# Kernel tuning notes

Hardware: AMD Instinct MI355X
Metric: run time of the kernel (lower is better)

The kernel has to match this reference:

```python
import jax, jax.numpy as jnp
import numpy as np

B, S, D, H = 1, 2048, 1024, 16
HD = D // H  # head_dim = 64
ROPE_BASE = 10000.0


def setup_inputs() -> dict:
    key = jax.random.key(0)
    k1, k2, k3, k4, k5 = jax.random.split(key, 5)
    std = 0.02
    return {
        "hidden_states": jax.random.normal(k1, (B, S, D), dtype=jnp.float32),
        "attention_mask": jnp.ones((B, S), dtype=jnp.int32),
        "position_ids": jnp.broadcast_to(jnp.arange(S, dtype=jnp.int32), (B, S)),
        "wq": jax.random.normal(k2, (D, D), dtype=jnp.float32) * std,
        "wk": jax.random.normal(k3, (D, D), dtype=jnp.float32) * std,
        "wv": jax.random.normal(k4, (D, D), dtype=jnp.float32) * std,
        "wo": jax.random.normal(k5, (D, D), dtype=jnp.float32) * std,
    }


def _rope_cos_sin(position_ids):
    # standard llama freqs: 1/base^(2i/hd), interleaved-pair rotation
    inv_freq = 1.0 / (ROPE_BASE ** (jnp.arange(0, HD, 2, dtype=jnp.float32) / HD))  # [HD/2]
    freqs = position_ids.astype(jnp.float32)[..., None] * inv_freq  # [B,S,HD/2]
    # add head axis for broadcasting: [B,S,1,HD/2]
    return jnp.cos(freqs)[:, :, None, :], jnp.sin(freqs)[:, :, None, :]


def _apply_rope(x, cos, sin):
    # x: [B,S,H,HD]; pairs (x0,x1) rotated as complex (x0+i*x1)*(cos+i*sin)
    x2 = x.reshape(x.shape[:-1] + (HD // 2, 2))
    x0, x1 = x2[..., 0], x2[..., 1]
    out = jnp.stack([x0 * cos - x1 * sin, x0 * sin + x1 * cos], axis=-1)
    return out.reshape(x.shape)


def _attention(hidden_states, attention_mask, position_ids, wq, wk, wv, wo):
    xq = (hidden_states @ wq).reshape(B, S, H, HD)
    xk = (hidden_states @ wk).reshape(B, S, H, HD)
    xv = (hidden_states @ wv).reshape(B, S, H, HD)

    cos, sin = _rope_cos_sin(position_ids)
    xq = _apply_rope(xq, cos, sin)
    xk = _apply_rope(xk, cos, sin)

    # combined causal + padding mask -> additive bias
    causal = jnp.tril(jnp.ones((S, S), dtype=bool))[None, None]  # [1,1,S,S]
    pad = (attention_mask > 0)[:, None, None, :]  # [B,1,1,S]
    mask = jnp.logical_and(causal, pad)
    neg = jnp.finfo(jnp.float32).min
    bias = jnp.where(mask, 0.0, neg).astype(jnp.float32)

    scale = 1.0 / np.sqrt(HD).astype(np.float32)
    scores = jnp.einsum("bqhd,bkhd->bhqk", xq, xk) * scale + bias  # [B,H,S,S]
    attn_weights = jax.nn.softmax(scores, axis=-1)

    attn_output = jnp.einsum("bhqk,bkhd->bqhd", attn_weights, xv)
    attn_output = attn_output.reshape(B, S, D)
    return attn_output @ wo


def reference(hidden_states, attention_mask, position_ids, wq, wk, wv, wo):
    return _attention(hidden_states, attention_mask, position_ids, wq, wk, wv, wo)
```

## Files before the change

kernel.cpp:

```cpp
#include <hip/hip_runtime.h>
#include <stdint.h>

#define SEQ 2048
#define DMODEL 1024
#define NHEAD 16
#define HDIM 64
#define KCH 256
#define NCH 8
#define NITEMS 576
#define WPH 512

typedef unsigned short u16;
typedef __attribute__((ext_vector_type(4))) float f32x4;
typedef __attribute__((ext_vector_type(8))) __bf16 bf16x8;
typedef __attribute__((ext_vector_type(8))) u16 u16x8;

__device__ __forceinline__ u16 f2bf(float f) {
  unsigned int u = __builtin_bit_cast(unsigned int, f);
  unsigned int r = (u + 0x7FFFu + ((u >> 16) & 1u)) >> 16;
  return (u16)r;
}
__device__ __forceinline__ float bf2f(u16 b) {
  unsigned int u = ((unsigned int)b) << 16;
  return __builtin_bit_cast(float, u);
}
__device__ __forceinline__ bf16x8 load8(const u16* p) {
  return __builtin_bit_cast(bf16x8, *(const u16x8*)p);
}
__device__ __forceinline__ void gl_lds16(const void* g, void* l) {
  __builtin_amdgcn_global_load_lds(
      (const __attribute__((address_space(1))) unsigned int*)g,
      (__attribute__((address_space(3))) unsigned int*)l, 16, 0, 0);
}

__global__ __launch_bounds__(256) void convert_x(const float* __restrict__ X,
                                                 u16* __restrict__ Xb) {
  int i = (blockIdx.x * 256 + threadIdx.x) * 4;
  float4 v = *(const float4*)(X + i);
  union { u16 s[4]; uint2 u; } o;
  o.s[0] = f2bf(v.x); o.s[1] = f2bf(v.y); o.s[2] = f2bf(v.z); o.s[3] = f2bf(v.w);
  *(uint2*)(Xb + i) = o.u;
}

__global__ __launch_bounds__(256) void transpose_w(
    const float* __restrict__ W0, const float* __restrict__ W1,
    const float* __restrict__ W2, const float* __restrict__ W3,
    u16* __restrict__ T0, u16* __restrict__ T1,
    u16* __restrict__ T2, u16* __restrict__ T3) {
  __shared__ u16 tile[64][65];
  int bz = blockIdx.z;
  const float* W = bz == 0 ? W0 : bz == 1 ? W1 : bz == 2 ? W2 : W3;
  u16* T = bz == 0 ? T0 : bz == 1 ? T1 : bz == 2 ? T2 : T3;
  int n0 = blockIdx.x * 64, k0 = blockIdx.y * 64;
  int t = threadIdx.x;
#pragma unroll 4
  for (int i = 0; i < 16; ++i) {
    int idx = i * 256 + t;
    int r = idx >> 6, c = idx & 63;
    tile[r][c] = f2bf(W[(k0 + r) * 1024 + n0 + c]);
  }
  __syncthreads();
#pragma unroll 4
  for (int i = 0; i < 16; ++i) {
    int idx = i * 256 + t;
    int r = idx >> 6, c = idx & 63;
    T[(n0 + r) * 1024 + k0 + c] = tile[c][r];
  }
}

template <int BM, int BN, int NMATS, bool OUTF32>
__global__ __launch_bounds__(256) void gemm_bf16(
    const u16* __restrict__ A, const u16* __restrict__ B0,
    const u16* __restrict__ B1, const u16* __restrict__ B2,
    u16* __restrict__ O0, u16* __restrict__ O1, u16* __restrict__ O2,
    float* __restrict__ OF) {
  constexpr int MI = BM / 32, NI = BN / 32;
  constexpr int LA = BM / 64, LB = BN / 64;
  __shared__ u16 As[BM * 32];
  __shared__ u16 Bs[BN * 32];
  const int t = threadIdx.x;
  const int lane = t & 63, w = t >> 6;
  const int g = lane >> 4, li = lane & 15;
  const int n0g = blockIdx.x * BN;
  const int mat = n0g >> 10;
  const int n0 = n0g & 1023;
  const u16* Bp = (NMATS == 1 || mat == 0) ? B0 : (mat == 1 ? B1 : B2);
  const int m0 = blockIdx.y * BM;
  const int wm = (w >> 1) * (BM / 2), wn = (w & 1) * (BN / 2);
  f32x4 acc[MI][NI] = {};
  for (int k0 = 0; k0 < 1024; k0 += 32) {
#pragma unroll
    for (int it = 0; it < LA; ++it) {
      int L = it * 2048 + t * 8;
      int r = L >> 5, c = L & 31;
      gl_lds16(A + (m0 + r) * 1024 + k0 + c, (char*)As + it * 4096 + w * 1024);
    }
#pragma unroll
    for (int it = 0; it < LB; ++it) {
      int L = it * 2048 + t * 8;
      int r = L >> 5, c = L & 31;
      gl_lds16(Bp + (n0 + r) * 1024 + k0 + c, (char*)Bs + it * 4096 + w * 1024);
    }
    __syncthreads();
    bf16x8 af[MI], bfr[NI];
#pragma unroll
    for (int mi = 0; mi < MI; ++mi) af[mi] = load8(&As[(wm + mi * 16 + li) * 32 + g * 8]);
#pragma unroll
    for (int ni = 0; ni < NI; ++ni) bfr[ni] = load8(&Bs[(wn + ni * 16 + li) * 32 + g * 8]);
#pragma unroll
    for (int mi = 0; mi < MI; ++mi)
#pragma unroll
      for (int ni = 0; ni < NI; ++ni)
        acc[mi][ni] = __builtin_amdgcn_mfma_f32_16x16x32_bf16(af[mi], bfr[ni], acc[mi][ni], 0, 0, 0);
    __syncthreads();
  }
  u16* Ob = (NMATS == 1 || mat == 0) ? O0 : (mat == 1 ? O1 : O2);
#pragma unroll
  for (int mi = 0; mi < MI; ++mi)
#pragma unroll
    for (int ni = 0; ni < NI; ++ni)
#pragma unroll
      for (int r = 0; r < 4; ++r) {
        int m = m0 + wm + mi * 16 + g * 4 + r;
        int n = n0 + wn + ni * 16 + li;
        float v = acc[mi][ni][r];
        if (OUTF32) OF[m * 1024 + n] = v;
        else Ob[m * 1024 + n] = f2bf(v);
      }
}

__global__ __launch_bounds__(256) void rope_qk(u16* __restrict__ Qb, u16* __restrict__ Kb,
                                               const int* __restrict__ pos_ids) {
  int gid = blockIdx.x * 256 + threadIdx.x;
  int s = gid >> 9;
  int rem = gid & 511;
  int h = rem >> 5, i = rem & 31;
  float pos = (float)pos_ids[s];
  float inv = exp2f(-(float)i * (13.287712379549449f / 32.0f));
  float ang = pos * inv;
  float sn, cs;
  sincosf(ang, &sn, &cs);
  int base = s * 1024 + h * 64 + 2 * i;
  {
    float x0 = bf2f(Qb[base]), x1 = bf2f(Qb[base + 1]);
    Qb[base]     = f2bf((x0 * cs - x1 * sn) * 0.125f);
    Qb[base + 1] = f2bf((x0 * sn + x1 * cs) * 0.125f);
  }
  {
    float x0 = bf2f(Kb[base]), x1 = bf2f(Kb[base + 1]);
    Kb[base]     = f2bf(x0 * cs - x1 * sn);
    Kb[base + 1] = f2bf(x0 * sn + x1 * cs);
  }
}

__global__ __launch_bounds__(256) void v_transpose(const u16* __restrict__ Vb,
                                                   u16* __restrict__ Vt) {
  __shared__ u16 tile[64][65];
  const int t = threadIdx.x;
  const int s0 = blockIdx.x * 64, h = blockIdx.y;
#pragma unroll 4
  for (int i = 0; i < 16; ++i) {
    int idx = i * 256 + t;
    int r = idx >> 6, c = idx & 63;
    tile[r][c] = Vb[(s0 + r) * 1024 + h * 64 + c];
  }
  __syncthreads();
#pragma unroll 4
  for (int i = 0; i < 16; ++i) {
    int idx = i * 256 + t;
    int d = idx >> 6, sc = idx & 63;
    Vt[h * (64 * 2048) + d * 2048 + s0 + sc] = tile[sc][d];
  }
}

__global__ __launch_bounds__(256) void attn_partial(
    const u16* __restrict__ Qb, const u16* __restrict__ Kb,
    const u16* __restrict__ Vt, const int* __restrict__ amask,
    float* __restrict__ Mpart, float* __restrict__ Lpart, u16* __restrict__ Opart) {
  const int t = threadIdx.x, lane = t & 63, w = t >> 6;
  const int g = lane >> 4, li = lane & 15;
  const int bid = blockIdx.x;
  const int h = bid & 15;
  const int wih = (bid >> 4) * 4 + w;
  __shared__ u16 Plds[4][16][40];
  const u16* Vh = Vt + h * (64 * 2048);
  for (int j = wih; j < NITEMS; j += WPH) {
    int c = (j >= 560) ? 7 : (j >= 528) ? 6 : (j >= 480) ? 5 : (j >= 416) ? 4
          : (j >= 336) ? 3 : (j >= 240) ? 2 : (j >= 128) ? 1 : 0;
    int qb = 16 * c + (j - (128 * c - 8 * c * (c - 1)));
    const int qb16 = qb * 16;
    const int kstart = c * KCH;
    const int kend = min(kstart + KCH, qb16 + 16);
    bf16x8 qf0 = load8(Qb + (qb16 + li) * 1024 + h * 64 + 0 + g * 8);
    bf16x8 qf1 = load8(Qb + (qb16 + li) * 1024 + h * 64 + 32 + g * 8);
    f32x4 acc[4] = {};
    float mrow[4] = {-1e30f, -1e30f, -1e30f, -1e30f};
    float lrow[4] = {0.f, 0.f, 0.f, 0.f};
    for (int k0 = kstart; k0 < kend; k0 += 32) {
      f32x4 sc[2] = {};
#pragma unroll
      for (int sub = 0; sub < 2; ++sub) {
        bf16x8 kf0 = load8(Kb + (k0 + sub * 16 + li) * 1024 + h * 64 + 0 + g * 8);
        bf16x8 kf1 = load8(Kb + (k0 + sub * 16 + li) * 1024 + h * 64 + 32 + g * 8);
        sc[sub] = __builtin_amdgcn_mfma_f32_16x16x32_bf16(qf0, kf0, sc[sub], 0, 0, 0);
        sc[sub] = __builtin_amdgcn_mfma_f32_16x16x32_bf16(qf1, kf1, sc[sub], 0, 0, 0);
      }
      float sv[2][4];
      float tmax[4] = {-1e30f, -1e30f, -1e30f, -1e30f};
#pragma unroll
      for (int sub = 0; sub < 2; ++sub) {
        int key = k0 + sub * 16 + li;
        bool kok = (amask[key] != 0);
#pragma unroll
        for (int r = 0; r < 4; ++r) {
          int q = qb16 + g * 4 + r;
          float v = (kok && key <= q) ? sc[sub][r] : -1e30f;
          sv[sub][r] = v;
          tmax[r] = fmaxf(tmax[r], v);
        }
      }
#pragma unroll
      for (int m = 1; m < 16; m <<= 1)
#pragma unroll
        for (int r = 0; r < 4; ++r) tmax[r] = fmaxf(tmax[r], __shfl_xor(tmax[r], m, 64));
      float alpha[4];
#pragma unroll
      for (int r = 0; r < 4; ++r) {
        float mn = fmaxf(mrow[r], tmax[r]);
        alpha[r] = __expf(mrow[r] - mn);
        mrow[r] = mn;
      }
      float ps[4] = {0.f, 0.f, 0.f, 0.f};
#pragma unroll
      for (int sub = 0; sub < 2; ++sub)
#pragma unroll
        for (int r = 0; r < 4; ++r) {
          float p = __expf(sv[sub][r] - mrow[r]);
          ps[r] += p;
          Plds[w][g * 4 + r][sub * 16 + li] = f2bf(p);
        }
#pragma unroll
      for (int m = 1; m < 16; m <<= 1)
#pragma unroll
        for (int r = 0; r < 4; ++r) ps[r] += __shfl_xor(ps[r], m, 64);
#pragma unroll
      for (int r = 0; r < 4; ++r) lrow[r] = lrow[r] * alpha[r] + ps[r];
#pragma unroll
      for (int ti = 0; ti < 4; ++ti)
#pragma unroll
        for (int r = 0; r < 4; ++r) acc[ti][r] *= alpha[r];
      bf16x8 pf = load8(&Plds[w][li][g * 8]);
#pragma unroll
      for (int ti = 0; ti < 4; ++ti) {
        bf16x8 vf = load8(Vh + (ti * 16 + li) * 2048 + k0 + g * 8);
        acc[ti] = __builtin_amdgcn_mfma_f32_16x16x32_bf16(pf, vf, acc[ti], 0, 0, 0);
      }
    }
    const int idx = (h * 128 + qb) * NCH + c;
    if (li == 0) {
#pragma unroll
      for (int r = 0; r < 4; ++r) {
        Mpart[idx * 16 + g * 4 + r] = mrow[r];
        Lpart[idx * 16 + g * 4 + r] = lrow[r];
      }
    }
#pragma unroll
    for (int ti = 0; ti < 4; ++ti)
#pragma unroll
      for (int r = 0; r < 4; ++r)
        Opart[idx * 1024 + (g * 4 + r) * 64 + ti * 16 + li] = f2bf(acc[ti][r]);
  }
}

__global__ __launch_bounds__(256) void attn_combine(
    const float* __restrict__ Mpart, const float* __restrict__ Lpart,
    const u16* __restrict__ Opart, u16* __restrict__ Ab) {
  const int qb = blockIdx.x, h = blockIdx.y;
  const int t = threadIdx.x;
  const int q = t >> 4, dg = t & 15;
  const int nch = qb / 16 + 1;
  const int base = (h * 128 + qb) * NCH;
  float M = -1e30f;
#pragma unroll
  for (int c = 0; c < NCH; ++c)
    if (c < nch) M = fmaxf(M, Mpart[(base + c) * 16 + q]);
  float L = 0.f;
  float o[4] = {0.f, 0.f, 0.f, 0.f};
#pragma unroll
  for (int c = 0; c < NCH; ++c)
    if (c < nch) {
      float e = __expf(Mpart[(base + c) * 16 + q] - M);
      L += e * Lpart[(base + c) * 16 + q];
      const u16* op = Opart + (base + c) * 1024 + q * 64 + dg * 4;
      uint2 pk = *(const uint2*)op;
      const u16* ps = (const u16*)&pk;
#pragma unroll
      for (int j = 0; j < 4; ++j) o[j] += e * bf2f(ps[j]);
    }
  float inv = 1.f / L;
  u16* dst = Ab + (qb * 16 + q) * 1024 + h * 64 + dg * 4;
  union { u16 s[4]; uint2 u; } ou;
#pragma unroll
  for (int j = 0; j < 4; ++j) ou.s[j] = f2bf(o[j] * inv);
  *(uint2*)dst = ou.u;
}

extern "C" void kernel_launch(void* const* d_in, const int* in_sizes, int n_in,
                              void* d_out, int out_size, void* d_ws, size_t ws_size,
                              hipStream_t stream) {
  const float* X = (const float*)d_in[0];
  const int* amask = (const int*)d_in[1];
  const int* pos = (const int*)d_in[2];
  const float* wq = (const float*)d_in[3];
  const float* wk = (const float*)d_in[4];
  const float* wv = (const float*)d_in[5];
  const float* wo = (const float*)d_in[6];
  float* out = (float*)d_out;
  char* ws = (char*)d_ws;
  u16* Xb  = (u16*)(ws);
  u16* Wtq = (u16*)(ws + (4u  << 20));
  u16* Wtk = (u16*)(ws + (6u  << 20));
  u16* Wtv = (u16*)(ws + (8u  << 20));
  u16* Wto = (u16*)(ws + (10u << 20));
  u16* Qb  = (u16*)(ws + (12u << 20));
  u16* Kb  = (u16*)(ws + (16u << 20));
  u16* Vb  = (u16*)(ws + (20u << 20));
  u16* Vt  = (u16*)(ws + (24u << 20));
  u16* Ab  = (u16*)(ws + (28u << 20));
  float* Mpart = (float*)(ws + (32u << 20));
  float* Lpart = (float*)(ws + (33u << 20));
  u16*   Opart = (u16*)(ws + (34u << 20));

  convert_x<<<2048, 256, 0, stream>>>(X, Xb);
  transpose_w<<<dim3(16, 16, 4), 256, 0, stream>>>(wq, wk, wv, wo, Wtq, Wtk, Wtv, Wto);
  gemm_bf16<64, 128, 3, false><<<dim3(24, 32), 256, 0, stream>>>(Xb, Wtq, Wtk, Wtv, Qb, Kb, Vb, nullptr);
  rope_qk<<<4096, 256, 0, stream>>>(Qb, Kb, pos);
  v_transpose<<<dim3(32, 16), 256, 0, stream>>>(Vb, Vt);
  attn_partial<<<2048, 256, 0, stream>>>(Qb, Kb, Vt, amask, Mpart, Lpart, Opart);
  attn_combine<<<dim3(128, 16), 256, 0, stream>>>(Mpart, Lpart, Opart, Ab);
  gemm_bf16<64, 64, 1, true><<<dim3(16, 32), 256, 0, stream>>>(Ab, Wto, nullptr, nullptr,
                                                               nullptr, nullptr, nullptr, out);
}
```

Measured before the change: 145.6 us.

## Widen attention work items to 32 queries and 64-key steps for K/V reuse

```diff
diff --git a/kernel.cpp b/kernel.cpp
--- a/kernel.cpp
+++ b/kernel.cpp
@@ -7,8 +7,7 @@
 #define HDIM 64
 #define KCH 256
 #define NCH 8
-#define NITEMS 576
-#define WPH 512
+#define NIT32 288
 
 typedef unsigned short u16;
 typedef __attribute__((ext_vector_type(4))) float f32x4;
@@ -181,95 +180,136 @@
   const int g = lane >> 4, li = lane & 15;
   const int bid = blockIdx.x;
   const int h = bid & 15;
-  const int wih = (bid >> 4) * 4 + w;
-  __shared__ u16 Plds[4][16][40];
+  const int j = (bid >> 4) * 4 + w;
+  __shared__ u16 Plds[4][2][16][72];
   const u16* Vh = Vt + h * (64 * 2048);
-  for (int j = wih; j < NITEMS; j += WPH) {
-    int c = (j >= 560) ? 7 : (j >= 528) ? 6 : (j >= 480) ? 5 : (j >= 416) ? 4
-          : (j >= 336) ? 3 : (j >= 240) ? 2 : (j >= 128) ? 1 : 0;
-    int qb = 16 * c + (j - (128 * c - 8 * c * (c - 1)));
-    const int qb16 = qb * 16;
-    const int kstart = c * KCH;
-    const int kend = min(kstart + KCH, qb16 + 16);
-    bf16x8 qf0 = load8(Qb + (qb16 + li) * 1024 + h * 64 + 0 + g * 8);
-    bf16x8 qf1 = load8(Qb + (qb16 + li) * 1024 + h * 64 + 32 + g * 8);
-    f32x4 acc[4] = {};
-    float mrow[4] = {-1e30f, -1e30f, -1e30f, -1e30f};
-    float lrow[4] = {0.f, 0.f, 0.f, 0.f};
-    for (int k0 = kstart; k0 < kend; k0 += 32) {
-      f32x4 sc[2] = {};
-#pragma unroll
-      for (int sub = 0; sub < 2; ++sub) {
-        bf16x8 kf0 = load8(Kb + (k0 + sub * 16 + li) * 1024 + h * 64 + 0 + g * 8);
-        bf16x8 kf1 = load8(Kb + (k0 + sub * 16 + li) * 1024 + h * 64 + 32 + g * 8);
-        sc[sub] = __builtin_amdgcn_mfma_f32_16x16x32_bf16(qf0, kf0, sc[sub], 0, 0, 0);
-        sc[sub] = __builtin_amdgcn_mfma_f32_16x16x32_bf16(qf1, kf1, sc[sub], 0, 0, 0);
-      }
-      float sv[2][4];
-      float tmax[4] = {-1e30f, -1e30f, -1e30f, -1e30f};
-#pragma unroll
-      for (int sub = 0; sub < 2; ++sub) {
-        int key = k0 + sub * 16 + li;
-        bool kok = (amask[key] != 0);
+  const int c = (j >= 280) ? 7 : (j >= 264) ? 6 : (j >= 240) ? 5 : (j >= 208) ? 4
+              : (j >= 168) ? 3 : (j >= 120) ? 2 : (j >= 64) ? 1 : 0;
+  const int qb = 8 * c + (j - (64 * c - 4 * c * (c - 1)));
+  const int q0 = qb * 32;
+  const int kstart = c * KCH;
+  const int kend = min(kstart + KCH, q0 + 32);
+  bf16x8 qf[2][2];
+#pragma unroll
+  for (int a = 0; a < 2; ++a)
+#pragma unroll
+    for (int hf = 0; hf < 2; ++hf)
+      qf[a][hf] = load8(Qb + (q0 + a * 16 + li) * 1024 + h * 64 + hf * 32 + g * 8);
+  f32x4 acc[2][4] = {};
+  float mrow[2][4], lrow[2][4];
+#pragma unroll
+  for (int a = 0; a < 2; ++a)
+#pragma unroll
+    for (int r = 0; r < 4; ++r) { mrow[a][r] = -1e30f; lrow[a][r] = 0.f; }
+  for (int k0 = kstart; k0 < kend; k0 += 64) {
+    f32x4 sc[2][4] = {};
+#pragma unroll
+    for (int s = 0; s < 4; ++s) {
+      bf16x8 kf0 = load8(Kb + (k0 + s * 16 + li) * 1024 + h * 64 + 0 + g * 8);
+      bf16x8 kf1 = load8(Kb + (k0 + s * 16 + li) * 1024 + h * 64 + 32 + g * 8);
+#pragma unroll
+      for (int a = 0; a < 2; ++a) {
+        sc[a][s] = __builtin_amdgcn_mfma_f32_16x16x32_bf16(qf[a][0], kf0, sc[a][s], 0, 0, 0);
+        sc[a][s] = __builtin_amdgcn_mfma_f32_16x16x32_bf16(qf[a][1], kf1, sc[a][s], 0, 0, 0);
+      }
+    }
+    float sv[2][4][4];
+    float tmax[2][4];
+#pragma unroll
+    for (int a = 0; a < 2; ++a)
+#pragma unroll
+      for (int r = 0; r < 4; ++r) tmax[a][r] = -1e30f;
+#pragma unroll
+    for (int s = 0; s < 4; ++s) {
+      int key = k0 + s * 16 + li;
+      bool kok = (amask[key] != 0);
+#pragma unroll
+      for (int a = 0; a < 2; ++a)
 #pragma unroll
         for (int r = 0; r < 4; ++r) {
-          int q = qb16 + g * 4 + r;
-          float v = (kok && key <= q) ? sc[sub][r] : -1e30f;
-          sv[sub][r] = v;
-          tmax[r] = fmaxf(tmax[r], v);
+          int q = q0 + a * 16 + g * 4 + r;
+          float v = (kok && key <= q) ? sc[a][s][r] : -1e30f;
+          sv[a][s][r] = v;
+          tmax[a][r] = fmaxf(tmax[a][r], v);
         }
-      }
-#pragma unroll
-      for (int m = 1; m < 16; m <<= 1)
-#pragma unroll
-        for (int r = 0; r < 4; ++r) tmax[r] = fmaxf(tmax[r], __shfl_xor(tmax[r], m, 64));
-      float alpha[4];
+    }
+#pragma unroll
+    for (int m = 1; m < 16; m <<= 1)
+#pragma unroll
+      for (int a = 0; a < 2; ++a)
+#pragma unroll
+        for (int r = 0; r < 4; ++r)
+          tmax[a][r] = fmaxf(tmax[a][r], __shfl_xor(tmax[a][r], m, 64));
+    float alpha[2][4];
+#pragma unroll
+    for (int a = 0; a < 2; ++a)
 #pragma unroll
       for (int r = 0; r < 4; ++r) {
-        float mn = fmaxf(mrow[r], tmax[r]);
-        alpha[r] = __expf(mrow[r] - mn);
-        mrow[r] = mn;
-      }
-      float ps[4] = {0.f, 0.f, 0.f, 0.f};
-#pragma unroll
-      for (int sub = 0; sub < 2; ++sub)
+        float mn = fmaxf(mrow[a][r], tmax[a][r]);
+        alpha[a][r] = __expf(mrow[a][r] - mn);
+        mrow[a][r] = mn;
+      }
+    float ps[2][4] = {};
+#pragma unroll
+    for (int s = 0; s < 4; ++s)
+#pragma unroll
+      for (int a = 0; a < 2; ++a)
 #pragma unroll
         for (int r = 0; r < 4; ++r) {
-          float p = __expf(sv[sub][r] - mrow[r]);
-          ps[r] += p;
-          Plds[w][g * 4 + r][sub * 16 + li] = f2bf(p);
+          float p = __expf(sv[a][s][r] - mrow[a][r]);
+          ps[a][r] += p;
+          Plds[w][a][g * 4 + r][s * 16 + li] = f2bf(p);
         }
 #pragma unroll
-      for (int m = 1; m < 16; m <<= 1)
-#pragma unroll
-        for (int r = 0; r < 4; ++r) ps[r] += __shfl_xor(ps[r], m, 64);
-#pragma unroll
-      for (int r = 0; r < 4; ++r) lrow[r] = lrow[r] * alpha[r] + ps[r];
+    for (int m = 1; m < 16; m <<= 1)
+#pragma unroll
+      for (int a = 0; a < 2; ++a)
+#pragma unroll
+        for (int r = 0; r < 4; ++r) ps[a][r] += __shfl_xor(ps[a][r], m, 64);
+#pragma unroll
+    for (int a = 0; a < 2; ++a)
+#pragma unroll
+      for (int r = 0; r < 4; ++r) lrow[a][r] = lrow[a][r] * alpha[a][r] + ps[a][r];
+#pragma unroll
+    for (int a = 0; a < 2; ++a)
 #pragma unroll
       for (int ti = 0; ti < 4; ++ti)
 #pragma unroll
-        for (int r = 0; r < 4; ++r) acc[ti][r] *= alpha[r];
-      bf16x8 pf = load8(&Plds[w][li][g * 8]);
-#pragma unroll
-      for (int ti = 0; ti < 4; ++ti) {
-        bf16x8 vf = load8(Vh + (ti * 16 + li) * 2048 + k0 + g * 8);
-        acc[ti] = __builtin_amdgcn_mfma_f32_16x16x32_bf16(pf, vf, acc[ti], 0, 0, 0);
-      }
-    }
-    const int idx = (h * 128 + qb) * NCH + c;
-    if (li == 0) {
+        for (int r = 0; r < 4; ++r) acc[a][ti][r] *= alpha[a][r];
+    bf16x8 pf[2][2];
+#pragma unroll
+    for (int a = 0; a < 2; ++a)
+#pragma unroll
+      for (int ks = 0; ks < 2; ++ks)
+        pf[a][ks] = load8(&Plds[w][a][li][ks * 32 + g * 8]);
+#pragma unroll
+    for (int ti = 0; ti < 4; ++ti) {
+      bf16x8 vf0 = load8(Vh + (ti * 16 + li) * 2048 + k0 + 0 + g * 8);
+      bf16x8 vf1 = load8(Vh + (ti * 16 + li) * 2048 + k0 + 32 + g * 8);
+#pragma unroll
+      for (int a = 0; a < 2; ++a) {
+        acc[a][ti] = __builtin_amdgcn_mfma_f32_16x16x32_bf16(pf[a][0], vf0, acc[a][ti], 0, 0, 0);
+        acc[a][ti] = __builtin_amdgcn_mfma_f32_16x16x32_bf16(pf[a][1], vf1, acc[a][ti], 0, 0, 0);
+      }
+    }
+  }
+  const int idx = (h * 64 + qb) * NCH + c;
+  if (li == 0) {
+#pragma unroll
+    for (int a = 0; a < 2; ++a)
 #pragma unroll
       for (int r = 0; r < 4; ++r) {
-        Mpart[idx * 16 + g * 4 + r] = mrow[r];
-        Lpart[idx * 16 + g * 4 + r] = lrow[r];
-      }
-    }
+        Mpart[idx * 32 + a * 16 + g * 4 + r] = mrow[a][r];
+        Lpart[idx * 32 + a * 16 + g * 4 + r] = lrow[a][r];
+      }
+  }
+#pragma unroll
+  for (int a = 0; a < 2; ++a)
 #pragma unroll
     for (int ti = 0; ti < 4; ++ti)
 #pragma unroll
       for (int r = 0; r < 4; ++r)
-        Opart[idx * 1024 + (g * 4 + r) * 64 + ti * 16 + li] = f2bf(acc[ti][r]);
-  }
+        Opart[idx * 2048 + (a * 16 + g * 4 + r) * 64 + ti * 16 + li] = f2bf(acc[a][ti][r]);
 }
 
 __global__ __launch_bounds__(256) void attn_combine(
@@ -277,32 +317,31 @@
     const u16* __restrict__ Opart, u16* __restrict__ Ab) {
   const int qb = blockIdx.x, h = blockIdx.y;
   const int t = threadIdx.x;
-  const int q = t >> 4, dg = t & 15;
-  const int nch = qb / 16 + 1;
-  const int base = (h * 128 + qb) * NCH;
+  const int q = t >> 3, dg = t & 7;
+  const int nch = qb / 8 + 1;
+  const int base = (h * 64 + qb) * NCH;
   float M = -1e30f;
 #pragma unroll
   for (int c = 0; c < NCH; ++c)
-    if (c < nch) M = fmaxf(M, Mpart[(base + c) * 16 + q]);
+    if (c < nch) M = fmaxf(M, Mpart[(base + c) * 32 + q]);
   float L = 0.f;
-  float o[4] = {0.f, 0.f, 0.f, 0.f};
+  float o[8] = {};
 #pragma unroll
   for (int c = 0; c < NCH; ++c)
     if (c < nch) {
-      float e = __expf(Mpart[(base + c) * 16 + q] - M);
-      L += e * Lpart[(base + c) * 16 + q];
-      const u16* op = Opart + (base + c) * 1024 + q * 64 + dg * 4;
-      uint2 pk = *(const uint2*)op;
+      float e = __expf(Mpart[(base + c) * 32 + q] - M);
+      L += e * Lpart[(base + c) * 32 + q];
+      uint4 pk = *(const uint4*)(Opart + (base + c) * 2048 + q * 64 + dg * 8);
       const u16* ps = (const u16*)&pk;
 #pragma unroll
-      for (int j = 0; j < 4; ++j) o[j] += e * bf2f(ps[j]);
+      for (int jj = 0; jj < 8; ++jj) o[jj] += e * bf2f(ps[jj]);
     }
   float inv = 1.f / L;
-  u16* dst = Ab + (qb * 16 + q) * 1024 + h * 64 + dg * 4;
-  union { u16 s[4]; uint2 u; } ou;
-#pragma unroll
-  for (int j = 0; j < 4; ++j) ou.s[j] = f2bf(o[j] * inv);
-  *(uint2*)dst = ou.u;
+  u16* dst = Ab + (qb * 32 + q) * 1024 + h * 64 + dg * 8;
+  union { u16 s[8]; uint4 u; } ou;
+#pragma unroll
+  for (int jj = 0; jj < 8; ++jj) ou.s[jj] = f2bf(o[jj] * inv);
+  *(uint4*)dst = ou.u;
 }
 
 extern "C" void kernel_launch(void* const* d_in, const int* in_sizes, int n_in,
@@ -336,8 +375,8 @@
   gemm_bf16<64, 128, 3, false><<<dim3(24, 32), 256, 0, stream>>>(Xb, Wtq, Wtk, Wtv, Qb, Kb, Vb, nullptr);
   rope_qk<<<4096, 256, 0, stream>>>(Qb, Kb, pos);
   v_transpose<<<dim3(32, 16), 256, 0, stream>>>(Vb, Vt);
-  attn_partial<<<2048, 256, 0, stream>>>(Qb, Kb, Vt, amask, Mpart, Lpart, Opart);
-  attn_combine<<<dim3(128, 16), 256, 0, stream>>>(Mpart, Lpart, Opart, Ab);
+  attn_partial<<<1152, 256, 0, stream>>>(Qb, Kb, Vt, amask, Mpart, Lpart, Opart);
+  attn_combine<<<dim3(64, 16), 256, 0, stream>>>(Mpart, Lpart, Opart, Ab);
   gemm_bf16<64, 64, 1, true><<<dim3(16, 32), 256, 0, stream>>>(Ab, Wto, nullptr, nullptr,
                                                                nullptr, nullptr, nullptr, out);
 }
```

Result: faster. 117.2 us (-19.5%).
